# Performance work log

Hardware: AMD Instinct MI355X
Metric: run time of the kernel (lower is better)

The kernel has to match this reference:

```python
import jax, jax.numpy as jnp
import numpy as np

MAX_PERIOD = 10000.0


def _rope(x, ts):
    # x: [B,H,T,D], ts: [B,T] integer positions (per-batch offset + arange(T))
    B, H, T, D = x.shape
    half = D // 2
    freqs = jnp.exp(jnp.arange(half, dtype=jnp.float32) * (-np.log(MAX_PERIOD) * 2.0 / D))
    ang = ts.astype(jnp.float32)[:, None, :, None] * freqs  # [B,1,T,half]
    cos, sin = jnp.cos(ang), jnp.sin(ang)
    xr = x.reshape(B, H, T, half, 2)  # interleaved (real, imag) pairs
    r, i = xr[..., 0], xr[..., 1]
    out = jnp.stack([r * cos - i * sin, r * sin + i * cos], axis=-1)
    return out.reshape(B, H, T, D)


def setup_inputs() -> dict:
    key = jax.random.key(0)
    ks = jax.random.split(key, 7)
    B, T, C = 8, 128, 1024
    H, D, CAP = 16, 64, 2048
    return {
        'x': jax.random.normal(ks[0], (B, T, C), dtype=jnp.float32),
        'w_in': jax.random.normal(ks[1], (3 * C, C), dtype=jnp.float32) * 0.02,
        'w_out': jax.random.normal(ks[2], (C, C), dtype=jnp.float32) * 0.02,
        'cache_k': jax.random.normal(ks[3], (B, H, CAP, D), dtype=jnp.float32),
        'cache_v': jax.random.normal(ks[4], (B, H, CAP, D), dtype=jnp.float32),
        'end_offset': jax.random.randint(ks[5], (B,), 0, CAP).astype(jnp.int64) if jax.config.jax_enable_x64 else jax.random.randint(ks[5], (B,), 0, CAP),
        'exec_mask': jnp.ones((B,), dtype=bool),
    }


def reference(x, w_in, w_out, cache_k, cache_v, end_offset, exec_mask):
    B, T, C = x.shape
    H, CAP = cache_k.shape[1], cache_k.shape[2]
    D = C // H
    context = CAP  # capacity == self.context

    # fused in-projection, split per rearrange 'b t (p h d) -> p b h t d', p=3
    qkv = (x @ w_in.T).reshape(B, T, 3, H, D).transpose(2, 0, 3, 1, 4)
    q, k, v = qkv[0], qkv[1], qkv[2]  # each [B,H,T,D]

    ts = end_offset[:, None] + jnp.arange(T)  # [B,T] absolute positions of new tokens
    q = _rope(q, ts)
    k = _rope(k, ts)

    # ring-buffer scatter (RingKVCache.complete)
    idx = ts % CAP  # [B,T]
    bI = jnp.arange(B)[:, None, None]
    hI = jnp.arange(H)[None, :, None]
    cache_k = cache_k.at[bI, hI, idx[:, None, :]].set(k)
    cache_v = cache_v.at[bI, hI, idx[:, None, :]].set(v)

    # absolute position of every cache slot, -1 for invalid slots
    cap_idx = jnp.arange(CAP)
    last = end_offset + T - 1  # [B]
    end_index = last % CAP
    delta = cap_idx[None, :] - end_index[:, None]  # [B,CAP]
    positions = jnp.where(delta <= 0, last[:, None] + delta, last[:, None] + delta - CAP)
    new_end = jnp.where(exec_mask, end_offset + T, end_offset)
    positions = jnp.where(cap_idx[None, :] >= new_end[:, None], -1, positions)

    # causal + context mask derived from positions
    d = ts[:, :, None] - positions[:, None, :]  # [B,T,CAP]
    mask = (positions[:, None, :] >= 0) & (d >= 0) & (d < context)

    scale = 1.0 / np.sqrt(D)
    scores = jnp.einsum('bhtd,bhsd->bhts', q, cache_k) * scale  # [B,H,T,CAP]
    scores = jnp.where(mask[:, None], scores, jnp.asarray(-1e9, scores.dtype))
    attn = jax.nn.softmax(scores, axis=-1)
    out = jnp.einsum('bhts,bhsd->bhtd', attn, cache_v)
    out = out.transpose(0, 2, 1, 3).reshape(B, T, C)  # 'b h t d -> b t (h d)'
    return out @ w_out.T
```

## Files before the change

### kernel.cpp

```cpp
#include <hip/hip_runtime.h>
#include <math.h>

#define BB 8
#define TT 128
#define CC 1024
#define HH 16
#define DD 64
#define CAP 2048

typedef __attribute__((ext_vector_type(8))) short short8;
typedef __attribute__((ext_vector_type(4))) short short4v;
typedef __attribute__((ext_vector_type(4))) float float4v;
typedef _Float16 half8 __attribute__((ext_vector_type(8)));
typedef _Float16 half4v __attribute__((ext_vector_type(4)));

__device__ __forceinline__ short f2bf(float x) {
    union { float f; unsigned u; } un; un.f = x;
    unsigned r = (un.u + 0x7FFF + ((un.u >> 16) & 1)) >> 16;
    return (short)r;
}
__device__ __forceinline__ float bf2f(unsigned short h) {
    union { unsigned u; float f; } un; un.u = ((unsigned)h) << 16;
    return un.f;
}

__global__ __launch_bounds__(256) void split_all(const float* __restrict__ x,
                                                 const float* __restrict__ w_in,
                                                 const float* __restrict__ w_out,
                                                 _Float16* __restrict__ xhi,
                                                 _Float16* __restrict__ xlo,
                                                 _Float16* __restrict__ wh,
                                                 _Float16* __restrict__ woh) {
    size_t i = ((size_t)blockIdx.x * 256 + threadIdx.x) * 4;
    if (i < (size_t)1048576) {
        float4 f = *(const float4*)(x + i);
        half4v h, l;
        h.x = (_Float16)f.x; l.x = (_Float16)(f.x - (float)h.x);
        h.y = (_Float16)f.y; l.y = (_Float16)(f.y - (float)h.y);
        h.z = (_Float16)f.z; l.z = (_Float16)(f.z - (float)h.z);
        h.w = (_Float16)f.w; l.w = (_Float16)(f.w - (float)h.w);
        *(half4v*)(xhi + i) = h;
        *(half4v*)(xlo + i) = l;
    } else if (i < (size_t)4194304) {
        size_t off = i - 1048576;
        float4 f = *(const float4*)(w_in + off);
        half4v h;
        h.x = (_Float16)f.x; h.y = (_Float16)f.y; h.z = (_Float16)f.z; h.w = (_Float16)f.w;
        *(half4v*)(wh + off) = h;
    } else {
        size_t off = i - 4194304;
        float4 f = *(const float4*)(w_out + off);
        half4v h;
        h.x = (_Float16)f.x; h.y = (_Float16)f.y; h.z = (_Float16)f.z; h.w = (_Float16)f.w;
        *(half4v*)(woh + off) = h;
    }
}

template <int ROWS>
__device__ __forceinline__ void stage_glds(const unsigned short* __restrict__ src,
                                           unsigned short* lds, int K, int wv, int lane) {
#pragma unroll
    for (int c = wv; c < ROWS / 16; c += 4) {
        int row = c * 16 + (lane >> 2);
        int g = lane & 3;
        const unsigned short* ga = src + (size_t)row * K + g * 8;
        unsigned short* la = lds + c * 512 + lane * 8;
        __builtin_amdgcn_global_load_lds((__attribute__((address_space(1))) const unsigned short*)ga,
                                         (__attribute__((address_space(3))) unsigned short*)la,
                                         16, 0, 0);
    }
}

template <int MT, int NT>
__global__ __launch_bounds__(256) void gemm_f16x2(const _Float16* __restrict__ Ahi,
                                                  const _Float16* __restrict__ Alo,
                                                  const _Float16* __restrict__ Bh,
                                                  float* __restrict__ C, int M, int N, int K) {
    constexpr int BM = 2 * MT * 16, BN = 2 * NT * 16;
    __shared__ __align__(16) _Float16 As_h[BM * 32];
    __shared__ __align__(16) _Float16 As_l[BM * 32];
    __shared__ __align__(16) _Float16 Bs[BN * 32];

    int tid = threadIdx.x;
    int lane = tid & 63, wv = tid >> 6;
    int wr = wv >> 1, wc = wv & 1;
    int quad = lane >> 4, lq = lane & 15;
    int m0 = blockIdx.y * BM, n0 = blockIdx.x * BN;

    float4v acc[MT][NT];
#pragma unroll
    for (int mt = 0; mt < MT; ++mt)
#pragma unroll
        for (int nt = 0; nt < NT; ++nt) acc[mt][nt] = (float4v){0.f, 0.f, 0.f, 0.f};

    const unsigned short* a_h = (const unsigned short*)(Ahi + (size_t)m0 * K);
    const unsigned short* a_l = (const unsigned short*)(Alo + (size_t)m0 * K);
    const unsigned short* b_h = (const unsigned short*)(Bh + (size_t)n0 * K);

    for (int k0 = 0; k0 < K; k0 += 32) {
        __syncthreads();
        stage_glds<BM>(a_h + k0, (unsigned short*)As_h, K, wv, lane);
        stage_glds<BM>(a_l + k0, (unsigned short*)As_l, K, wv, lane);
        stage_glds<BN>(b_h + k0, (unsigned short*)Bs, K, wv, lane);
        __syncthreads();

        half8 ah[MT], al[MT];
#pragma unroll
        for (int mt = 0; mt < MT; ++mt) {
            int row = wr * MT * 16 + mt * 16 + lq;
            ah[mt] = *(const half8*)&As_h[row * 32 + quad * 8];
            al[mt] = *(const half8*)&As_l[row * 32 + quad * 8];
        }
#pragma unroll
        for (int nt = 0; nt < NT; ++nt) {
            int row = wc * NT * 16 + nt * 16 + lq;
            half8 bh = *(const half8*)&Bs[row * 32 + quad * 8];
#pragma unroll
            for (int mt = 0; mt < MT; ++mt) {
                float4v c = acc[mt][nt];
                c = __builtin_amdgcn_mfma_f32_16x16x32_f16(ah[mt], bh, c, 0, 0, 0);
                c = __builtin_amdgcn_mfma_f32_16x16x32_f16(al[mt], bh, c, 0, 0, 0);
                acc[mt][nt] = c;
            }
        }
    }

#pragma unroll
    for (int mt = 0; mt < MT; ++mt)
#pragma unroll
        for (int nt = 0; nt < NT; ++nt) {
            int n = n0 + wc * NT * 16 + nt * 16 + lq;
#pragma unroll
            for (int r = 0; r < 4; ++r) {
                int m = m0 + wr * MT * 16 + mt * 16 + quad * 4 + r;
                C[(size_t)m * N + n] = acc[mt][nt][r];
            }
        }
}

__global__ __launch_bounds__(256) void rope_scatter(const float* __restrict__ qkv,
                                                    unsigned short* __restrict__ q_bf,
                                                    float* __restrict__ cache_k,
                                                    float* __restrict__ cache_v,
                                                    const int* __restrict__ end_offset) {
    int gid = blockIdx.x * 256 + threadIdx.x;
    int j = gid & 31;
    int h = (gid >> 5) & 15;
    int t = (gid >> 9) & 127;
    int b = gid >> 16;

    int ts = end_offset[b] + t;
    int slot = ts & (CAP - 1);

    float freq = expf(-0.28782313662425574f * (float)j);
    float ang = (float)ts * freq;
    float s, c;
    sincosf(ang, &s, &c);

    const float* base = qkv + (size_t)(b * TT + t) * (3 * CC);
    int col = h * DD + 2 * j;
    float2 qv = *(const float2*)&base[col];
    float2 kv = *(const float2*)&base[CC + col];
    float2 vv = *(const float2*)&base[2 * CC + col];

    float qr = qv.x * c - qv.y * s;
    float qi = qv.x * s + qv.y * c;
    float kr = kv.x * c - kv.y * s;
    float ki = kv.x * s + kv.y * c;

    size_t qo = ((size_t)(b * HH + h) * TT + t) * DD + 2 * j;
    ushort2 qp;
    qp.x = (unsigned short)f2bf(qr);
    qp.y = (unsigned short)f2bf(qi);
    *(ushort2*)&q_bf[qo] = qp;
    size_t ko = ((size_t)(b * HH + h) * CAP + slot) * DD + 2 * j;
    *(float2*)&cache_k[ko] = make_float2(kr, ki);
    *(float2*)&cache_v[ko] = vv;
}

__global__ __launch_bounds__(256) void attn_mfma(const unsigned short* __restrict__ qb,
                                                 const float* __restrict__ ck,
                                                 const float* __restrict__ cv,
                                                 const int* __restrict__ endo,
                                                 const unsigned char* __restrict__ emb,
                                                 const int* __restrict__ emi,
                                                 _Float16* __restrict__ ahi,
                                                 _Float16* __restrict__ alo) {
    __shared__ __align__(16) short k_s[64 * 72];
    __shared__ __align__(16) short v_t[64 * 64];
    __shared__ __align__(16) short p_s[4][16 * 72];
    __shared__ float stat_s[4][16];

    int tid = threadIdx.x;
    int lane = tid & 63, wv = tid >> 6;
    int quad = lane >> 4, lq = lane & 15;
    int hb = blockIdx.x;
    int h = hb & 15, b = hb >> 4;
    int qc2 = blockIdx.y;
    int qrow = qc2 * 64 + wv * 16 + lq;

    int end0 = endo[b];
    int em = (emb[b] != 0) || (emi[b] != 0);
    int last = end0 + TT - 1;
    int end_index = last & (CAP - 1);
    int new_end = em ? (end0 + TT) : end0;
    int se = new_end < CAP ? new_end : CAP;
    int ntiles = (se + 63) >> 6;

    const unsigned short* qrp = qb + ((size_t)(b * HH + h) * TT + qrow) * DD;
    short8 aq0 = *(const short8*)(qrp + quad * 8);
    short8 aq1 = *(const short8*)(qrp + 32 + quad * 8);

    const float* kg = ck + (size_t)(b * HH + h) * CAP * DD;
    const float* vg = cv + (size_t)(b * HH + h) * CAP * DD;

    int k_row = tid >> 4, k_f4 = tid & 15;
    float4 kreg[4];
    float vreg[2][8];

    float m[4], l[4];
#pragma unroll
    for (int r = 0; r < 4; ++r) { m[r] = -3.0e38f; l[r] = 0.f; }
    float4v acc[4];
#pragma unroll
    for (int mt = 0; mt < 4; ++mt) acc[mt] = (float4v){0.f, 0.f, 0.f, 0.f};

    if (ntiles > 0) {
#pragma unroll
        for (int i = 0; i < 4; ++i)
            kreg[i] = *(const float4*)&kg[(size_t)(k_row + 16 * i) * DD + k_f4 * 4];
#pragma unroll
        for (int gi = 0; gi < 2; ++gi) {
            int g = wv + gi * 4;
#pragma unroll
            for (int i = 0; i < 8; ++i)
                vreg[gi][i] = vg[(size_t)(g * 8 + i) * DD + lane];
        }
    }

    for (int t = 0; t < ntiles; ++t) {
        int s0 = t * 64;
        __syncthreads();
#pragma unroll
        for (int i = 0; i < 4; ++i) {
            float4 f = kreg[i];
            short4v sv;
            sv.x = f2bf(f.x); sv.y = f2bf(f.y); sv.z = f2bf(f.z); sv.w = f2bf(f.w);
            *(short4v*)&k_s[(k_row + 16 * i) * 72 + k_f4 * 4] = sv;
        }
#pragma unroll
        for (int gi = 0; gi < 2; ++gi) {
            int g = wv + gi * 4;
            short8 pk;
#pragma unroll
            for (int i = 0; i < 8; ++i) pk[i] = f2bf(vreg[gi][i]);
            *(short8*)&v_t[lane * 64 + (g ^ (lane & 7)) * 8] = pk;
        }
        __syncthreads();
        if (t + 1 < ntiles) {
            int sn = s0 + 64;
#pragma unroll
            for (int i = 0; i < 4; ++i)
                kreg[i] = *(const float4*)&kg[(size_t)(sn + k_row + 16 * i) * DD + k_f4 * 4];
#pragma unroll
            for (int gi = 0; gi < 2; ++gi) {
                int g = wv + gi * 4;
#pragma unroll
                for (int i = 0; i < 8; ++i)
                    vreg[gi][i] = vg[(size_t)(sn + g * 8 + i) * DD + lane];
            }
        }

        float4v sc[4];
#pragma unroll
        for (int nt = 0; nt < 4; ++nt) {
            const short* kr = &k_s[(nt * 16 + lq) * 72 + quad * 8];
            short8 bk0 = *(const short8*)kr;
            short8 bk1 = *(const short8*)(kr + 32);
            float4v c = (float4v){0.f, 0.f, 0.f, 0.f};
            c = __builtin_amdgcn_mfma_f32_16x16x32_bf16(aq0, bk0, c, 0, 0, 0);
            c = __builtin_amdgcn_mfma_f32_16x16x32_bf16(aq1, bk1, c, 0, 0, 0);
            sc[nt] = c;
        }

        float x[4][4];
#pragma unroll
        for (int nt = 0; nt < 4; ++nt) {
            int s = s0 + nt * 16 + lq;
            int delta = s - end_index;
            int pos = (delta <= 0) ? (last + delta) : (last + delta - CAP);
            if (s >= new_end) pos = -1;
#pragma unroll
            for (int r = 0; r < 4; ++r) {
                int tq = end0 + qc2 * 64 + wv * 16 + quad * 4 + r;
                int dd = tq - pos;
                bool valid = (pos >= 0) && (dd >= 0) && (dd < CAP);
                x[nt][r] = valid ? sc[nt][r] * 0.125f : -1.0e9f;
            }
        }
        float al[4];
#pragma unroll
        for (int r = 0; r < 4; ++r) {
            float vm = fmaxf(fmaxf(x[0][r], x[1][r]), fmaxf(x[2][r], x[3][r]));
            vm = fmaxf(vm, __shfl_xor(vm, 1, 64));
            vm = fmaxf(vm, __shfl_xor(vm, 2, 64));
            vm = fmaxf(vm, __shfl_xor(vm, 4, 64));
            vm = fmaxf(vm, __shfl_xor(vm, 8, 64));
            float mn = fmaxf(m[r], vm);
            al[r] = __expf(m[r] - mn);
            float ps = 0.f;
#pragma unroll
            for (int nt = 0; nt < 4; ++nt) {
                float p = __expf(x[nt][r] - mn);
                x[nt][r] = p;
                ps += p;
            }
            ps += __shfl_xor(ps, 1, 64);
            ps += __shfl_xor(ps, 2, 64);
            ps += __shfl_xor(ps, 4, 64);
            ps += __shfl_xor(ps, 8, 64);
            l[r] = l[r] * al[r] + ps;
            m[r] = mn;
        }
#pragma unroll
        for (int r = 0; r < 4; ++r)
#pragma unroll
            for (int nt = 0; nt < 4; ++nt)
                p_s[wv][(quad * 4 + r) * 72 + nt * 16 + lq] = f2bf(x[nt][r]);
        if (lq == 0) {
#pragma unroll
            for (int r = 0; r < 4; ++r) stat_s[wv][quad * 4 + r] = al[r];
        }

        float af = stat_s[wv][lq];
        short8 bp0 = *(const short8*)&p_s[wv][lq * 72 + quad * 8];
        short8 bp1 = *(const short8*)&p_s[wv][lq * 72 + 32 + quad * 8];
#pragma unroll
        for (int mt = 0; mt < 4; ++mt) {
            int d = mt * 16 + lq;
            const short* vr = &v_t[d * 64];
            short8 av0 = *(const short8*)(vr + ((quad ^ (d & 7)) * 8));
            short8 av1 = *(const short8*)(vr + (((4 + quad) ^ (d & 7)) * 8));
            float4v a = acc[mt];
            a.x *= af; a.y *= af; a.z *= af; a.w *= af;
            a = __builtin_amdgcn_mfma_f32_16x16x32_bf16(av0, bp0, a, 0, 0, 0);
            a = __builtin_amdgcn_mfma_f32_16x16x32_bf16(av1, bp1, a, 0, 0, 0);
            acc[mt] = a;
        }
    }

    if (lq == 0) {
#pragma unroll
        for (int r = 0; r < 4; ++r) stat_s[wv][quad * 4 + r] = l[r];
    }
    float lv = stat_s[wv][lq];
    float inv = (lv > 0.f) ? (1.f / lv) : 0.f;
    size_t obase = (size_t)(b * TT + qrow) * CC + h * DD;
#pragma unroll
    for (int mt = 0; mt < 4; ++mt) {
        half4v h4, l4;
        float o0 = acc[mt].x * inv, o1 = acc[mt].y * inv, o2 = acc[mt].z * inv, o3 = acc[mt].w * inv;
        h4.x = (_Float16)o0; l4.x = (_Float16)(o0 - (float)h4.x);
        h4.y = (_Float16)o1; l4.y = (_Float16)(o1 - (float)h4.y);
        h4.z = (_Float16)o2; l4.z = (_Float16)(o2 - (float)h4.z);
        h4.w = (_Float16)o3; l4.w = (_Float16)(o3 - (float)h4.w);
        *(half4v*)&ahi[obase + mt * 16 + quad * 4] = h4;
        *(half4v*)&alo[obase + mt * 16 + quad * 4] = l4;
    }
}

extern "C" void kernel_launch(void* const* d_in, const int* in_sizes, int n_in,
                              void* d_out, int out_size, void* d_ws, size_t ws_size,
                              hipStream_t stream) {
    const float* x = (const float*)d_in[0];
    const float* w_in = (const float*)d_in[1];
    const float* w_out = (const float*)d_in[2];
    float* cache_k = (float*)d_in[3];
    float* cache_v = (float*)d_in[4];
    const int* end_offset = (const int*)d_in[5];
    const unsigned char* exec_mask_b = (const unsigned char*)d_in[6];
    const int* exec_mask_i = (const int*)d_in[6];
    float* out = (float*)d_out;

    float* qkv = (float*)d_ws;
    unsigned short* q_bf = (unsigned short*)(qkv + (size_t)1024 * 3072);
    _Float16* xhi = (_Float16*)(q_bf + (size_t)1024 * 1024);
    _Float16* xlo = xhi + (size_t)1024 * 1024;
    _Float16* wh = xlo + (size_t)1024 * 1024;
    _Float16* woh = wh + (size_t)3072 * 1024;
    _Float16* ahi = woh + (size_t)1024 * 1024;
    _Float16* alo = ahi + (size_t)1024 * 1024;

    split_all<<<5120, 256, 0, stream>>>(x, w_in, w_out, xhi, xlo, wh, woh);
    gemm_f16x2<2, 4><<<dim3(3072 / 128, 1024 / 64), 256, 0, stream>>>(
        xhi, xlo, wh, qkv, BB * TT, 3 * CC, CC);
    rope_scatter<<<(BB * TT * HH * 32) / 256, 256, 0, stream>>>(qkv, q_bf, cache_k, cache_v, end_offset);
    attn_mfma<<<dim3(HH * BB, 2), 256, 0, stream>>>(q_bf, cache_k, cache_v, end_offset,
                                                    exec_mask_b, exec_mask_i, ahi, alo);
    gemm_f16x2<2, 2><<<dim3(1024 / 64, 1024 / 64), 256, 0, stream>>>(
        ahi, alo, woh, out, BB * TT, CC, CC);
}
```

Before: 254.0 us.

## Split attention over KV tiles across blocks and add combine kernel

The attention kernel now splits the KV tile loop into four chunks along a new grid dimension, so each block processes a quarter of the cache and writes unnormalised fp32 partial outputs plus per-row max and sum. A new combine kernel merges the partials with log-sum-exp rescaling and emits the hi/lo fp16 outputs. This raises the block count to fill the GPU and shorten the serial per-block loop, at the cost of extra partial-result memory traffic, an extra launch, and reuse of dead workspace buffers as scratch.

```diff
diff --git a/kernel.cpp b/kernel.cpp
--- a/kernel.cpp
+++ b/kernel.cpp
@@ -7,6 +7,7 @@
 #define HH 16
 #define DD 64
 #define CAP 2048
+#define NSPLIT 4
 
 typedef __attribute__((ext_vector_type(8))) short short8;
 typedef __attribute__((ext_vector_type(4))) short short4v;
@@ -184,8 +185,9 @@
                                                  const int* __restrict__ endo,
                                                  const unsigned char* __restrict__ emb,
                                                  const int* __restrict__ emi,
-                                                 _Float16* __restrict__ ahi,
-                                                 _Float16* __restrict__ alo) {
+                                                 float* __restrict__ pacc012,
+                                                 float* __restrict__ pacc3,
+                                                 float* __restrict__ pml) {
     __shared__ __align__(16) short k_s[64 * 72];
     __shared__ __align__(16) short v_t[64 * 64];
     __shared__ __align__(16) short p_s[4][16 * 72];
@@ -197,6 +199,7 @@
     int hb = blockIdx.x;
     int h = hb & 15, b = hb >> 4;
     int qc2 = blockIdx.y;
+    int sid = blockIdx.z;
     int qrow = qc2 * 64 + wv * 16 + lq;
 
     int end0 = endo[b];
@@ -206,6 +209,9 @@
     int new_end = em ? (end0 + TT) : end0;
     int se = new_end < CAP ? new_end : CAP;
     int ntiles = (se + 63) >> 6;
+    int tps = (ntiles + NSPLIT - 1) / NSPLIT;
+    int t0 = sid * tps;
+    int t1 = t0 + tps < ntiles ? t0 + tps : ntiles;
 
     const unsigned short* qrp = qb + ((size_t)(b * HH + h) * TT + qrow) * DD;
     short8 aq0 = *(const short8*)(qrp + quad * 8);
@@ -220,25 +226,26 @@
 
     float m[4], l[4];
 #pragma unroll
-    for (int r = 0; r < 4; ++r) { m[r] = -3.0e38f; l[r] = 0.f; }
+    for (int r = 0; r < 4; ++r) { m[r] = 0.0f; l[r] = 0.f; }
     float4v acc[4];
 #pragma unroll
     for (int mt = 0; mt < 4; ++mt) acc[mt] = (float4v){0.f, 0.f, 0.f, 0.f};
 
-    if (ntiles > 0) {
+    if (t0 < t1) {
+        int sb = t0 * 64;
 #pragma unroll
         for (int i = 0; i < 4; ++i)
-            kreg[i] = *(const float4*)&kg[(size_t)(k_row + 16 * i) * DD + k_f4 * 4];
+            kreg[i] = *(const float4*)&kg[(size_t)(sb + k_row + 16 * i) * DD + k_f4 * 4];
 #pragma unroll
         for (int gi = 0; gi < 2; ++gi) {
             int g = wv + gi * 4;
 #pragma unroll
             for (int i = 0; i < 8; ++i)
-                vreg[gi][i] = vg[(size_t)(g * 8 + i) * DD + lane];
-        }
-    }
-
-    for (int t = 0; t < ntiles; ++t) {
+                vreg[gi][i] = vg[(size_t)(sb + g * 8 + i) * DD + lane];
+        }
+    }
+
+    for (int t = t0; t < t1; ++t) {
         int s0 = t * 64;
         __syncthreads();
 #pragma unroll
@@ -257,7 +264,7 @@
             *(short8*)&v_t[lane * 64 + (g ^ (lane & 7)) * 8] = pk;
         }
         __syncthreads();
-        if (t + 1 < ntiles) {
+        if (t + 1 < t1) {
             int sn = s0 + 64;
 #pragma unroll
             for (int i = 0; i < 4; ++i)
@@ -295,7 +302,7 @@
                 int tq = end0 + qc2 * 64 + wv * 16 + quad * 4 + r;
                 int dd = tq - pos;
                 bool valid = (pos >= 0) && (dd >= 0) && (dd < CAP);
-                x[nt][r] = valid ? sc[nt][r] * 0.125f : -1.0e9f;
+                x[nt][r] = valid ? sc[nt][r] * 0.125f : -1.0e30f;
             }
         }
         float al[4];
@@ -349,24 +356,54 @@
         }
     }
 
+    int base_row = (b * HH + h) * TT + qc2 * 64;
+    float* pa = (sid < 3) ? (pacc012 + (size_t)sid * (16384 * 64)) : pacc3;
+    int row_g = base_row + wv * 16 + lq;
+#pragma unroll
+    for (int mt = 0; mt < 4; ++mt)
+        *(float4v*)&pa[(size_t)row_g * 64 + mt * 16 + quad * 4] = acc[mt];
     if (lq == 0) {
 #pragma unroll
-        for (int r = 0; r < 4; ++r) stat_s[wv][quad * 4 + r] = l[r];
-    }
-    float lv = stat_s[wv][lq];
-    float inv = (lv > 0.f) ? (1.f / lv) : 0.f;
-    size_t obase = (size_t)(b * TT + qrow) * CC + h * DD;
-#pragma unroll
-    for (int mt = 0; mt < 4; ++mt) {
-        half4v h4, l4;
-        float o0 = acc[mt].x * inv, o1 = acc[mt].y * inv, o2 = acc[mt].z * inv, o3 = acc[mt].w * inv;
-        h4.x = (_Float16)o0; l4.x = (_Float16)(o0 - (float)h4.x);
-        h4.y = (_Float16)o1; l4.y = (_Float16)(o1 - (float)h4.y);
-        h4.z = (_Float16)o2; l4.z = (_Float16)(o2 - (float)h4.z);
-        h4.w = (_Float16)o3; l4.w = (_Float16)(o3 - (float)h4.w);
-        *(half4v*)&ahi[obase + mt * 16 + quad * 4] = h4;
-        *(half4v*)&alo[obase + mt * 16 + quad * 4] = l4;
-    }
+        for (int r = 0; r < 4; ++r) {
+            int rg = base_row + wv * 16 + quad * 4 + r;
+            size_t ix = ((size_t)sid * 16384 + rg) * 2;
+            pml[ix] = m[r];
+            pml[ix + 1] = l[r];
+        }
+    }
+}
+
+__global__ __launch_bounds__(256) void attn_combine(const float* __restrict__ pacc012,
+                                                    const float* __restrict__ pacc3,
+                                                    const float* __restrict__ pml,
+                                                    _Float16* __restrict__ ahi,
+                                                    _Float16* __restrict__ alo) {
+    int gid = blockIdx.x * 256 + threadIdx.x;
+    int row = gid >> 6, d = gid & 63;
+
+    float mv[NSPLIT], lv[NSPLIT];
+#pragma unroll
+    for (int s = 0; s < NSPLIT; ++s) {
+        size_t ix = ((size_t)s * 16384 + row) * 2;
+        mv[s] = pml[ix];
+        lv[s] = pml[ix + 1];
+    }
+    float M = fmaxf(fmaxf(mv[0], mv[1]), fmaxf(mv[2], mv[3]));
+    float O = 0.f, L = 0.f;
+#pragma unroll
+    for (int s = 0; s < NSPLIT; ++s) {
+        const float* pa = (s < 3) ? (pacc012 + (size_t)s * (16384 * 64)) : pacc3;
+        float w = __expf(mv[s] - M);
+        L += w * lv[s];
+        O += w * pa[(size_t)row * 64 + d];
+    }
+    float o = (L > 0.f) ? (O / L) : 0.f;
+
+    int b = row >> 11, h = (row >> 7) & 15, q = row & 127;
+    size_t ob = ((size_t)(b * TT + q)) * CC + h * DD + d;
+    _Float16 hi = (_Float16)o;
+    ahi[ob] = hi;
+    alo[ob] = (_Float16)(o - (float)hi);
 }
 
 extern "C" void kernel_launch(void* const* d_in, const int* in_sizes, int n_in,
@@ -391,12 +428,18 @@
     _Float16* ahi = woh + (size_t)1024 * 1024;
     _Float16* alo = ahi + (size_t)1024 * 1024;
 
+    float* pacc012 = qkv;
+    float* pacc3 = (float*)xhi;
+    float* pml = (float*)wh;
+
     split_all<<<5120, 256, 0, stream>>>(x, w_in, w_out, xhi, xlo, wh, woh);
     gemm_f16x2<2, 4><<<dim3(3072 / 128, 1024 / 64), 256, 0, stream>>>(
         xhi, xlo, wh, qkv, BB * TT, 3 * CC, CC);
     rope_scatter<<<(BB * TT * HH * 32) / 256, 256, 0, stream>>>(qkv, q_bf, cache_k, cache_v, end_offset);
-    attn_mfma<<<dim3(HH * BB, 2), 256, 0, stream>>>(q_bf, cache_k, cache_v, end_offset,
-                                                    exec_mask_b, exec_mask_i, ahi, alo);
+    attn_mfma<<<dim3(HH * BB, 2, NSPLIT), 256, 0, stream>>>(q_bf, cache_k, cache_v, end_offset,
+                                                            exec_mask_b, exec_mask_i,
+                                                            pacc012, pacc3, pml);
+    attn_combine<<<(16384 * 64) / 256, 256, 0, stream>>>(pacc012, pacc3, pml, ahi, alo);
     gemm_f16x2<2, 2><<<dim3(1024 / 64, 1024 / 64), 256, 0, stream>>>(
         ahi, alo, woh, out, BB * TT, CC, CC);
 }
```

New measurement: 239.0 us. -5.9%, faster.
